# Optimization experiments

Measured on AMD Instinct MI355X. Metric: run time of the kernel, lower is better.

## Reference

```python
import jax, jax.numpy as jnp
import numpy as np

B, T, D = 2, 2048, 2048
H, DH, DR, DL = 16, 128, 64, 512
WINDOW, STRIDE, GLOBAL = 512, 64, 128
BASE, MAX_SEQ, ORIG_MAX = 10000.0, 131072, 4096
BETA_FAST, BETA_SLOW = 32.0, 1.0
SCALE = 1.0 / np.sqrt(DH)
SCALE_ROPE = 1.0 / np.sqrt(DR)


def _yarn_inv_freq():
    base_inv = 1.0 / (BASE ** (np.arange(0, DR, 2, dtype=np.float32) / DR))
    scale = MAX_SEQ / ORIG_MAX
    freqs = np.arange(DR // 2, dtype=np.float32)
    ramp = np.clip((freqs - BETA_SLOW) / (BETA_FAST - BETA_SLOW), 0.0, 1.0)
    return jnp.asarray(base_inv * (1 - ramp) + (base_inv / scale) * ramp)

_INV_FREQ = _yarn_inv_freq()
_YARN_FACTOR = np.float32(0.1 * np.log(MAX_SEQ / ORIG_MAX) + 1.0)


def _apply_rope(x):
    # x: [B, H, T, DR]
    t = jnp.arange(x.shape[2], dtype=jnp.float32)
    fr = t[:, None] * _INV_FREQ[None, :]            # [T, DR/2]
    emb = jnp.concatenate([fr, fr], axis=-1)        # [T, DR]
    cos, sin = jnp.cos(emb), jnp.sin(emb)
    x1, x2 = jnp.split(x, 2, axis=-1)
    rot = jnp.concatenate([-x2, x1], axis=-1)
    return (x * cos + rot * sin) * _YARN_FACTOR


def _sparse_mask(seq_len):
    pos = jnp.arange(seq_len)
    qp, kp = pos[:, None], pos[None, :]
    dist = qp - kp
    half = WINDOW // 2
    window = (dist >= -half) & (dist <= half)
    dilated = (kp % STRIDE == 0) | (kp < GLOBAL)
    causal = kp <= qp
    return (window | dilated) & causal              # [T, T] bool


def setup_inputs() -> dict:
    key = jax.random.key(0)
    ks = jax.random.split(key, 9)
    s = 0.02
    return {
        "x": jax.random.normal(ks[0], (B, T, D), jnp.float32),
        "w_q": jax.random.normal(ks[1], (D, D), jnp.float32) * s,
        "w_dkv": jax.random.normal(ks[2], (D, DL), jnp.float32) * s,
        "w_uk": jax.random.normal(ks[3], (DL, D), jnp.float32) * s,
        "w_uv": jax.random.normal(ks[4], (DL, D), jnp.float32) * s,
        "w_q_pos": jax.random.normal(ks[5], (D, H * DR), jnp.float32) * s,
        "w_k_pos": jax.random.normal(ks[6], (D, H * DR), jnp.float32) * s,
        "w_o": jax.random.normal(ks[7], (D, D), jnp.float32) * s,
    }


def reference(x, w_q, w_dkv, w_uk, w_uv, w_q_pos, w_k_pos, w_o):
    b, t, _ = x.shape
    # MLA projections
    q_c = (x @ w_q).reshape(b, t, H, DH).transpose(0, 2, 1, 3)      # [B,H,T,DH]
    c_kv = x @ w_dkv                                                # [B,T,DL]
    k_c = (c_kv @ w_uk).reshape(b, t, H, DH).transpose(0, 2, 1, 3)
    v_c = (c_kv @ w_uv).reshape(b, t, H, DH).transpose(0, 2, 1, 3)
    # decoupled RoPE branch (YaRN)
    q_r = (x @ w_q_pos).reshape(b, t, H, DR).transpose(0, 2, 1, 3)
    k_r = (x @ w_k_pos).reshape(b, t, H, DR).transpose(0, 2, 1, 3)
    q_r = _apply_rope(q_r)
    k_r = _apply_rope(k_r)
    # combined content + positional scores
    scores = jnp.einsum("bhqd,bhkd->bhqk", q_c, k_c) * SCALE \
           + jnp.einsum("bhqr,bhkr->bhqk", q_r, k_r) * SCALE_ROPE
    mask = _sparse_mask(t)                                          # [T,T]
    scores = jnp.where(mask[None, None], scores, -jnp.inf)
    attn = jax.nn.softmax(scores, axis=-1)
    out = jnp.einsum("bhqk,bhkd->bhqd", attn, v_c)                  # [B,H,T,DH]
    out = out.transpose(0, 2, 1, 3).reshape(b, t, D)
    return out @ w_o
```

## Files before the change

kernel.cpp:

```cpp
#include <hip/hip_runtime.h>
#include <hip/hip_bf16.h>
#include <cstdint>

typedef __attribute__((ext_vector_type(8))) short short8_t;
typedef __attribute__((ext_vector_type(4))) short short4_t;
typedef __attribute__((ext_vector_type(4))) float f32x4_t;

#define AS1 __attribute__((address_space(1)))
#define AS3 __attribute__((address_space(3)))

__device__ __forceinline__ void gload_lds16(const void* g, void* l) {
  __builtin_amdgcn_global_load_lds((const AS1 void*)g, (AS3 void*)l, 16, 0, 0);
}

__device__ __forceinline__ short8_t ld8(const __hip_bfloat16* p) {
  return *(const short8_t*)p;
}

__global__ __launch_bounds__(256) void k_prep(
    const float* __restrict__ x, __hip_bfloat16* __restrict__ xb,
    const float* __restrict__ wq,  const float* __restrict__ wqp,
    const float* __restrict__ wkp, const float* __restrict__ wdkv,
    const float* __restrict__ wuk, const float* __restrict__ wuv,
    const float* __restrict__ wo,
    __hip_bfloat16* __restrict__ Bt1, __hip_bfloat16* __restrict__ Bt2,
    __hip_bfloat16* __restrict__ woT) {
  __shared__ float t[64][65];
  int bid = blockIdx.x;
  if (bid < 4096) {
    int i = (bid * 256 + threadIdx.x) * 8;
    union { short8_t v; __hip_bfloat16 h[8]; } u;
#pragma unroll
    for (int j = 0; j < 8; ++j) u.h[j] = __float2bfloat16(x[i + j]);
    *(short8_t*)(xb + i) = u.v;
    return;
  }
  bid -= 4096;
  const float* in; __hip_bfloat16* out; int R, C, tile;
  if (bid < 1024)      { in = wq;   out = Bt1;                 R = 2048; C = 2048; tile = bid; }
  else if (bid < 1536) { in = wqp;  out = Bt1 + 2048UL * 2048; R = 2048; C = 1024; tile = bid - 1024; }
  else if (bid < 2048) { in = wkp;  out = Bt1 + 3072UL * 2048; R = 2048; C = 1024; tile = bid - 1536; }
  else if (bid < 2304) { in = wdkv; out = Bt1 + 4096UL * 2048; R = 2048; C = 512;  tile = bid - 2048; }
  else if (bid < 2560) { in = wuk;  out = Bt2;                 R = 512;  C = 2048; tile = bid - 2304; }
  else if (bid < 2816) { in = wuv;  out = Bt2 + 2048UL * 512;  R = 512;  C = 2048; tile = bid - 2560; }
  else                 { in = wo;   out = woT;                 R = 2048; C = 2048; tile = bid - 2816; }
  int nct = C >> 6;
  int ct = tile % nct, rt = tile / nct;
  int r0 = rt << 6, c0 = ct << 6;
#pragma unroll
  for (int i = 0; i < 16; ++i) {
    int idx = i * 256 + threadIdx.x;
    int r = idx >> 6, c = idx & 63;
    t[r][c] = in[(size_t)(r0 + r) * C + c0 + c];
  }
  __syncthreads();
#pragma unroll
  for (int i = 0; i < 16; ++i) {
    int idx = i * 256 + threadIdx.x;
    int c = idx >> 6, r = idx & 63;
    out[(size_t)(c0 + c) * R + r0 + r] = __float2bfloat16(t[r][c]);
  }
}

template<int MODE>
__global__ __launch_bounds__(256) void k_gemm2(const __hip_bfloat16* __restrict__ A,
                                               const __hip_bfloat16* __restrict__ Bt,
                                               int K, int nbx,
                                               void* __restrict__ O0, void* __restrict__ O1,
                                               void* __restrict__ O2, void* __restrict__ O3,
                                               float alpha) {
  __shared__ __align__(16) __hip_bfloat16 Al[3][128 * 32];
  __shared__ __align__(16) __hip_bfloat16 Bl[3][128 * 32];
  int bx = blockIdx.x % nbx, by = blockIdx.x / nbx;
  int tid = threadIdx.x, lane = tid & 63, w = tid >> 6;
  int L = lane & 15, hi = lane >> 4;
  int wr = (w >> 1) << 6, wc = (w & 1) << 6;
  f32x4_t acc[4][4] = {};
  const __hip_bfloat16* Ag = A + (size_t)(by * 128) * K;
  const __hip_bfloat16* Bg = Bt + (size_t)(bx * 128) * K;
  int rA = w * 16 + (lane >> 2);
  int cA = ((lane & 3) ^ ((lane >> 3) & 3)) * 8;
  int NT = K >> 5;

  auto stage = [&](int s) {
    int j = s % 3;
    int k0 = s << 5;
    gload_lds16(Ag + (size_t)rA * K + k0 + cA,        &Al[j][(w * 16) * 32]);
    gload_lds16(Ag + (size_t)(rA + 64) * K + k0 + cA, &Al[j][(64 + w * 16) * 32]);
    gload_lds16(Bg + (size_t)rA * K + k0 + cA,        &Bl[j][(w * 16) * 32]);
    gload_lds16(Bg + (size_t)(rA + 64) * K + k0 + cA, &Bl[j][(64 + w * 16) * 32]);
  };

  stage(0); stage(1);
  asm volatile("s_waitcnt vmcnt(4)\ns_barrier" ::: "memory");

  int hs = hi ^ ((L >> 1) & 3);
  for (int t = 0; t < NT; ++t) {
    int j = t % 3;
    short8_t af[4], bf[4];
#pragma unroll
    for (int m = 0; m < 4; ++m) af[m] = ld8(&Al[j][(wr + 16 * m + L) * 32 + 8 * hs]);
#pragma unroll
    for (int n = 0; n < 4; ++n) bf[n] = ld8(&Bl[j][(wc + 16 * n + L) * 32 + 8 * hs]);
    if (t + 2 < NT) stage(t + 2);
    __builtin_amdgcn_s_setprio(1);
#pragma unroll
    for (int m = 0; m < 4; ++m)
#pragma unroll
      for (int n = 0; n < 4; ++n)
        acc[m][n] = __builtin_amdgcn_mfma_f32_16x16x32_bf16(af[m], bf[n], acc[m][n], 0, 0, 0);
    __builtin_amdgcn_s_setprio(0);
    if (t + 2 < NT)      asm volatile("s_waitcnt vmcnt(4)\ns_barrier" ::: "memory");
    else if (t + 1 < NT) asm volatile("s_waitcnt vmcnt(0)\ns_barrier" ::: "memory");
  }

  int r0 = by * 128 + wr + 4 * hi;
  int cb = bx * 128 + wc;

  if (MODE == 1) {
    float* C = (float*)O0;
    size_t N = (size_t)nbx << 7;
#pragma unroll
    for (int m = 0; m < 4; ++m)
#pragma unroll
      for (int n = 0; n < 4; ++n)
#pragma unroll
        for (int i = 0; i < 4; ++i)
          C[(size_t)(r0 + 16 * m + i) * N + cb + 16 * n + L] = acc[m][n][i] * alpha;
  } else if (MODE == 2) {
    __hip_bfloat16* qcb = (__hip_bfloat16*)O0;
    __hip_bfloat16* qrb = (__hip_bfloat16*)O1;
    __hip_bfloat16* krb = (__hip_bfloat16*)O2;
    __hip_bfloat16* ckv = (__hip_bfloat16*)O3;
    if (bx < 16) {
      const float SCALE = 0.08838834764831845f;
#pragma unroll
      for (int m = 0; m < 4; ++m)
#pragma unroll
        for (int n = 0; n < 4; ++n)
#pragma unroll
          for (int i = 0; i < 4; ++i)
            qcb[(size_t)(r0 + 16 * m + i) * 2048 + cb + 16 * n + L] =
                __float2bfloat16(acc[m][n][i] * SCALE);
    } else if (bx < 32) {
      bool isq = bx < 24;
      __hip_bfloat16* dst = isq ? qrb : krb;
      float osc = isq ? 0.16832169878499666f : 1.3465735902799727f;
      int cbl = cb - (isq ? 2048 : 3072);
      float invf[2];
#pragma unroll
      for (int p = 0; p < 2; ++p) {
        float fi = (float)(16 * p + L);
        float bi = __expf(fi * -0.28782313662425574f);
        float ramp = fminf(fmaxf((fi - 1.0f) * (1.0f / 31.0f), 0.0f), 1.0f);
        invf[p] = bi * (1.0f - ramp * (31.0f / 32.0f));
      }
#pragma unroll
      for (int m = 0; m < 4; ++m)
#pragma unroll
        for (int i = 0; i < 4; ++i) {
          int row = r0 + 16 * m + i;
          float ft = (float)(row & 2047);
#pragma unroll
          for (int p = 0; p < 2; ++p) {
            float sn, cs;
            __sincosf(ft * invf[p], &sn, &cs);
            float x1 = acc[m][p][i], x2 = acc[m][p + 2][i];
            dst[(size_t)row * 1024 + cbl + 16 * p + L] =
                __float2bfloat16((x1 * cs - x2 * sn) * osc);
            dst[(size_t)row * 1024 + cbl + 32 + 16 * p + L] =
                __float2bfloat16((x2 * cs + x1 * sn) * osc);
          }
        }
    } else {
      int cbl = cb - 4096;
#pragma unroll
      for (int m = 0; m < 4; ++m)
#pragma unroll
        for (int n = 0; n < 4; ++n)
#pragma unroll
          for (int i = 0; i < 4; ++i)
            ckv[(size_t)(r0 + 16 * m + i) * 512 + cbl + 16 * n + L] =
                __float2bfloat16(acc[m][n][i]);
    }
  } else if (MODE == 3) {
    __hip_bfloat16* kcb = (__hip_bfloat16*)O0;
    __hip_bfloat16* vcb = (__hip_bfloat16*)O1;
    __hip_bfloat16* vT  = (__hip_bfloat16*)O2;
    if (bx < 16) {
#pragma unroll
      for (int m = 0; m < 4; ++m)
#pragma unroll
        for (int n = 0; n < 4; ++n)
#pragma unroll
          for (int i = 0; i < 4; ++i)
            kcb[(size_t)(r0 + 16 * m + i) * 2048 + cb + 16 * n + L] =
                __float2bfloat16(acc[m][n][i]);
    } else {
#pragma unroll
      for (int m = 0; m < 4; ++m)
#pragma unroll
        for (int n = 0; n < 4; ++n) {
          int vcol = cb - 2048 + 16 * n + L;
          int hh = vcol >> 7, dh = vcol & 127;
          int row0 = r0 + 16 * m;
          int b = row0 >> 11, t0 = row0 & 2047;
          union { short4_t v; __hip_bfloat16 h4[4]; } pk;
#pragma unroll
          for (int i = 0; i < 4; ++i) {
            __hip_bfloat16 bv = __float2bfloat16(acc[m][n][i]);
            vcb[(size_t)(row0 + i) * 2048 + vcol] = bv;
            pk.h4[i] = bv;
          }
          *(short4_t*)(vT + ((size_t)((b * 16 + hh) * 128 + dh) * 2048 + t0)) = pk.v;
        }
    }
  }
}

__global__ __launch_bounds__(256) void k_attn(const __hip_bfloat16* __restrict__ qc,
                                              const __hip_bfloat16* __restrict__ kc,
                                              const __hip_bfloat16* __restrict__ vcb,
                                              const __hip_bfloat16* __restrict__ qr,
                                              const __hip_bfloat16* __restrict__ kr,
                                              const __hip_bfloat16* __restrict__ vT,
                                              __hip_bfloat16* __restrict__ ao) {
  const int T = 2048;
  int bid = blockIdx.x;
  int xcd = bid & 7, r = bid >> 3;
  int jg = r >> 5;
  int qt = 31 - (r & 31);
  int bh = xcd + 8 * jg;
  int b = bh >> 4, h = bh & 15;
  int tid = threadIdx.x, lane = tid & 63, w = tid >> 6;
  int L = lane & 15, hi = lane >> 4;
  int q0 = qt * 64;

  __shared__ __align__(16) __hip_bfloat16 Kl[64 * 200];
  __shared__ __align__(16) __hip_bfloat16 Vt[128 * 64];
  __shared__ __align__(16) __hip_bfloat16 Pl[4][16 * 72];

  char* Vtb = (char*)Vt;
  const __hip_bfloat16* vTb = vT + (size_t)(b * 16 + h) * 128 * 2048;

  int qrow = q0 + w * 16 + L;
  size_t qb = (size_t)b * T + qrow;
  short8_t qf[6];
#pragma unroll
  for (int c = 0; c < 4; ++c)
    qf[c] = ld8(qc + qb * 2048 + h * 128 + 32 * c + 8 * hi);
#pragma unroll
  for (int c = 0; c < 2; ++c)
    qf[4 + c] = ld8(qr + qb * 1024 + h * 64 + 32 * c + 8 * hi);

  f32x4_t oacc[8] = {};
  float lpart[4] = {0.0f, 0.0f, 0.0f, 0.0f};

  int nd = qt - 6;

  for (int step = 0; step <= qt + 1; ++step) {
    bool compact = (step == qt + 1);
    if (compact && nd <= 0) break;
    int kt = step;
    if (!compact && kt > 1 && kt < qt - 4) continue;
    int k0 = kt * 64;

    if (!compact) {
#pragma unroll
      for (int i = 0; i < 6; ++i) {
        int ch = i * 256 + tid;
        int rr = ch / 24;
        int d = (ch % 24) * 8;
        size_t krow = (size_t)b * T + k0 + rr;
        const __hip_bfloat16* src = (d < 128)
            ? kc + krow * 2048 + h * 128 + d
            : kr + krow * 1024 + h * 64 + (d - 128);
        *(short8_t*)(Kl + rr * 200 + d) = ld8(src);
      }
#pragma unroll
      for (int i = 0; i < 4; ++i) {
        int ch = i * 256 + tid;
        int row = ch >> 3, c = ch & 7;
        int swc = c ^ (row & 7);
        *(short8_t*)(Vtb + row * 128 + 16 * swc) = ld8(vTb + (size_t)row * 2048 + k0 + c * 8);
      }
    } else {
#pragma unroll
      for (int i = 0; i < 6; ++i) {
        int ch = i * 256 + tid;
        int rr = ch / 24;
        int d = (ch % 24) * 8;
        int srcr = (rr < nd) ? 64 * (2 + rr) : 0;
        size_t krow = (size_t)b * T + srcr;
        const __hip_bfloat16* src = (d < 128)
            ? kc + krow * 2048 + h * 128 + d
            : kr + krow * 1024 + h * 64 + (d - 128);
        *(short8_t*)(Kl + rr * 200 + d) = ld8(src);
      }
#pragma unroll
      for (int i = 0; i < 2; ++i) {
        int ch = i * 256 + tid;
        int jj = ch >> 4, d0 = (ch & 15) * 8;
        if (jj < nd) {
          union { short8_t v; __hip_bfloat16 hh[8]; } u;
          u.v = ld8(vcb + (size_t)(b * 2048 + 64 * (2 + jj)) * 2048 + h * 128 + d0);
#pragma unroll
          for (int qq = 0; qq < 8; ++qq) {
            int dh = d0 + qq;
            int swc = (jj >> 3) ^ (dh & 7);
            *(__hip_bfloat16*)(Vtb + dh * 128 + 16 * swc + 2 * (jj & 7)) = u.hh[qq];
          }
        }
      }
    }
    __syncthreads();

    f32x4_t sacc[4] = {};
    __builtin_amdgcn_s_setprio(1);
#pragma unroll
    for (int n = 0; n < 4; ++n)
#pragma unroll
      for (int c = 0; c < 6; ++c) {
        short8_t bfr = ld8(Kl + (16 * n + L) * 200 + 32 * c + 8 * hi);
        sacc[n] = __builtin_amdgcn_mfma_f32_16x16x32_bf16(qf[c], bfr, sacc[n], 0, 0, 0);
      }
    __builtin_amdgcn_s_setprio(0);

    int rbase = q0 + w * 16 + 4 * hi;
#pragma unroll
    for (int n = 0; n < 4; ++n) {
      int col = L + 16 * n;
      int k = k0 + col;
#pragma unroll
      for (int i = 0; i < 4; ++i) {
        int rq = rbase + i;
        bool ok = compact ? (col < nd)
                          : ((k <= rq) && ((rq - k <= 256) || ((k & 63) == 0) || (k < 128)));
        float e = ok ? __expf(sacc[n][i]) : 0.0f;
        lpart[i] += e;
        Pl[w][(4 * hi + i) * 72 + 16 * n + L] = __float2bfloat16(e);
      }
    }

    __builtin_amdgcn_s_setprio(1);
#pragma unroll
    for (int ks = 0; ks < 2; ++ks) {
      short8_t pa = ld8(Pl[w] + L * 72 + 32 * ks + 8 * hi);
#pragma unroll
      for (int n = 0; n < 8; ++n) {
        int vrow = 16 * n + L;
        int chunk = (4 * ks + hi) ^ (vrow & 7);
        short8_t bv = *(const short8_t*)(Vtb + vrow * 128 + 16 * chunk);
        oacc[n] = __builtin_amdgcn_mfma_f32_16x16x32_bf16(pa, bv, oacc[n], 0, 0, 0);
      }
    }
    __builtin_amdgcn_s_setprio(0);
    __syncthreads();
  }

  for (int d = 1; d < 16; d <<= 1)
#pragma unroll
    for (int i = 0; i < 4; ++i) lpart[i] += __shfl_xor(lpart[i], d, 64);

#pragma unroll
  for (int n = 0; n < 8; ++n)
#pragma unroll
    for (int i = 0; i < 4; ++i) {
      int rq = q0 + w * 16 + 4 * hi + i;
      int cdh = 16 * n + L;
      float v = oacc[n][i] / lpart[i];
      ao[((size_t)b * T + rq) * 2048 + h * 128 + cdh] = __float2bfloat16(v);
    }
}

extern "C" void kernel_launch(void* const* d_in, const int* in_sizes, int n_in,
                              void* d_out, int out_size, void* d_ws, size_t ws_size,
                              hipStream_t stream) {
  const float* x     = (const float*)d_in[0];
  const float* w_q   = (const float*)d_in[1];
  const float* w_dkv = (const float*)d_in[2];
  const float* w_uk  = (const float*)d_in[3];
  const float* w_uv  = (const float*)d_in[4];
  const float* w_qp  = (const float*)d_in[5];
  const float* w_kp  = (const float*)d_in[6];
  const float* w_o   = (const float*)d_in[7];
  float* out = (float*)d_out;

  char* ws = (char*)d_ws;
  size_t off = 0;
  auto alloc = [&](size_t elems) {
    __hip_bfloat16* p = (__hip_bfloat16*)(ws + off);
    off += ((elems * 2 + 255) & ~(size_t)255);
    return p;
  };
  __hip_bfloat16* xb  = alloc(8388608);
  __hip_bfloat16* Bt1 = alloc(4608UL * 2048);
  __hip_bfloat16* Bt2 = alloc(4096UL * 512);
  __hip_bfloat16* woT = alloc(4194304);
  __hip_bfloat16* qcb = alloc(8388608);
  __hip_bfloat16* ckv = alloc(2097152);
  __hip_bfloat16* kcb = alloc(8388608);
  __hip_bfloat16* vcb = alloc(8388608);
  __hip_bfloat16* qrb = alloc(4194304);
  __hip_bfloat16* krb = alloc(4194304);
  __hip_bfloat16* aob = alloc(8388608);
  __hip_bfloat16* vT  = alloc(8388608);

  k_prep<<<7936, 256, 0, stream>>>(x, xb, w_q, w_qp, w_kp, w_dkv, w_uk, w_uv, w_o,
                                   Bt1, Bt2, woT);

  k_gemm2<2><<<36 * 32, 256, 0, stream>>>(xb, Bt1, 2048, 36, qcb, qrb, krb, ckv, 1.0f);
  k_gemm2<3><<<32 * 32, 256, 0, stream>>>(ckv, Bt2, 512, 32, kcb, vcb, vT, nullptr, 1.0f);

  k_attn<<<1024, 256, 0, stream>>>(qcb, kcb, vcb, qrb, krb, vT, aob);

  k_gemm2<1><<<16 * 32, 256, 0, stream>>>(aob, woT, 2048, 16, out, nullptr, nullptr, nullptr, 1.0f);
}
```

Measured before the change: 254.7 us.

## Use 256x256 tiles for projection GEMMs and split the c_kv GEMM out

Adds a k_gemm8 kernel with 512 threads and 256x256 output tiles, where each wave computes 128x64, and uses it for the fused Q/RoPE projection and the K/V up-projection. The c_kv down-projection is split into its own small 128x128-tile launch, so the big projection GEMM now covers an even 4096 columns. Larger tiles raise arithmetic intensity and cut redundant global loads of A and B. The cost is fewer blocks per launch (256), an extra kernel launch, more LDS and registers, and possible under-use of the GPU's CUs.

```diff
diff --git a/kernel.cpp b/kernel.cpp
--- a/kernel.cpp
+++ b/kernel.cpp
@@ -66,9 +66,7 @@
 __global__ __launch_bounds__(256) void k_gemm2(const __hip_bfloat16* __restrict__ A,
                                                const __hip_bfloat16* __restrict__ Bt,
                                                int K, int nbx,
-                                               void* __restrict__ O0, void* __restrict__ O1,
-                                               void* __restrict__ O2, void* __restrict__ O3,
-                                               float alpha) {
+                                               void* __restrict__ O0, float alpha) {
   __shared__ __align__(16) __hip_bfloat16 Al[3][128 * 32];
   __shared__ __align__(16) __hip_bfloat16 Bl[3][128 * 32];
   int bx = blockIdx.x % nbx, by = blockIdx.x / nbx;
@@ -115,35 +113,101 @@
   }
 
   int r0 = by * 128 + wr + 4 * hi;
-  int cb = bx * 128 + wc;
-
+  int c0 = bx * 128 + wc;
+  size_t N = (size_t)nbx << 7;
   if (MODE == 1) {
     float* C = (float*)O0;
-    size_t N = (size_t)nbx << 7;
 #pragma unroll
     for (int m = 0; m < 4; ++m)
 #pragma unroll
       for (int n = 0; n < 4; ++n)
 #pragma unroll
         for (int i = 0; i < 4; ++i)
-          C[(size_t)(r0 + 16 * m + i) * N + cb + 16 * n + L] = acc[m][n][i] * alpha;
-  } else if (MODE == 2) {
+          C[(size_t)(r0 + 16 * m + i) * N + c0 + 16 * n + L] = acc[m][n][i] * alpha;
+  } else {
+    __hip_bfloat16* C = (__hip_bfloat16*)O0;
+#pragma unroll
+    for (int m = 0; m < 4; ++m)
+#pragma unroll
+      for (int n = 0; n < 4; ++n)
+#pragma unroll
+        for (int i = 0; i < 4; ++i)
+          C[(size_t)(r0 + 16 * m + i) * N + c0 + 16 * n + L] =
+              __float2bfloat16(acc[m][n][i] * alpha);
+  }
+}
+
+template<int MODE>
+__global__ __launch_bounds__(512, 2) void k_gemm8(const __hip_bfloat16* __restrict__ A,
+                                                  const __hip_bfloat16* __restrict__ Bt,
+                                                  int K, int nbx,
+                                                  void* __restrict__ O0, void* __restrict__ O1,
+                                                  void* __restrict__ O2) {
+  __shared__ __align__(16) __hip_bfloat16 Al[3][256 * 32];
+  __shared__ __align__(16) __hip_bfloat16 Bl[3][256 * 32];
+  int bx = blockIdx.x % nbx, by = blockIdx.x / nbx;
+  int tid = threadIdx.x, lane = tid & 63, w = tid >> 6;
+  int L = lane & 15, hi = lane >> 4;
+  int wr = (w >> 2) << 7;
+  int wc = (w & 3) << 6;
+  f32x4_t acc[8][4] = {};
+  const __hip_bfloat16* Ag = A + (size_t)(by * 256) * K;
+  const __hip_bfloat16* Bg = Bt + (size_t)(bx * 256) * K;
+  int rA = w * 16 + (lane >> 2);
+  int cA = ((lane & 3) ^ ((lane >> 3) & 3)) * 8;
+  int NT = K >> 5;
+
+  auto stage = [&](int s) {
+    int j = s % 3;
+    int k0 = s << 5;
+    gload_lds16(Ag + (size_t)rA * K + k0 + cA,         &Al[j][(w * 16) * 32]);
+    gload_lds16(Ag + (size_t)(rA + 128) * K + k0 + cA, &Al[j][(128 + w * 16) * 32]);
+    gload_lds16(Bg + (size_t)rA * K + k0 + cA,         &Bl[j][(w * 16) * 32]);
+    gload_lds16(Bg + (size_t)(rA + 128) * K + k0 + cA, &Bl[j][(128 + w * 16) * 32]);
+  };
+
+  stage(0); stage(1);
+  asm volatile("s_waitcnt vmcnt(4)\ns_barrier" ::: "memory");
+
+  int hs = hi ^ ((L >> 1) & 3);
+  for (int t = 0; t < NT; ++t) {
+    int j = t % 3;
+    short8_t af[8], bf[4];
+#pragma unroll
+    for (int m = 0; m < 8; ++m) af[m] = ld8(&Al[j][(wr + 16 * m + L) * 32 + 8 * hs]);
+#pragma unroll
+    for (int n = 0; n < 4; ++n) bf[n] = ld8(&Bl[j][(wc + 16 * n + L) * 32 + 8 * hs]);
+    if (t + 2 < NT) stage(t + 2);
+    __builtin_amdgcn_s_setprio(1);
+#pragma unroll
+    for (int m = 0; m < 8; ++m)
+#pragma unroll
+      for (int n = 0; n < 4; ++n)
+        acc[m][n] = __builtin_amdgcn_mfma_f32_16x16x32_bf16(af[m], bf[n], acc[m][n], 0, 0, 0);
+    __builtin_amdgcn_s_setprio(0);
+    if (t + 2 < NT)      asm volatile("s_waitcnt vmcnt(4)\ns_barrier" ::: "memory");
+    else if (t + 1 < NT) asm volatile("s_waitcnt vmcnt(0)\ns_barrier" ::: "memory");
+  }
+
+  int r0 = by * 256 + wr + 4 * hi;
+  int cb = bx * 256 + wc;
+
+  if (MODE == 2) {
     __hip_bfloat16* qcb = (__hip_bfloat16*)O0;
     __hip_bfloat16* qrb = (__hip_bfloat16*)O1;
     __hip_bfloat16* krb = (__hip_bfloat16*)O2;
-    __hip_bfloat16* ckv = (__hip_bfloat16*)O3;
-    if (bx < 16) {
+    if (cb < 2048) {
       const float SCALE = 0.08838834764831845f;
 #pragma unroll
-      for (int m = 0; m < 4; ++m)
+      for (int m = 0; m < 8; ++m)
 #pragma unroll
         for (int n = 0; n < 4; ++n)
 #pragma unroll
           for (int i = 0; i < 4; ++i)
             qcb[(size_t)(r0 + 16 * m + i) * 2048 + cb + 16 * n + L] =
                 __float2bfloat16(acc[m][n][i] * SCALE);
-    } else if (bx < 32) {
-      bool isq = bx < 24;
+    } else {
+      bool isq = cb < 3072;
       __hip_bfloat16* dst = isq ? qrb : krb;
       float osc = isq ? 0.16832169878499666f : 1.3465735902799727f;
       int cbl = cb - (isq ? 2048 : 3072);
@@ -156,7 +220,7 @@
         invf[p] = bi * (1.0f - ramp * (31.0f / 32.0f));
       }
 #pragma unroll
-      for (int m = 0; m < 4; ++m)
+      for (int m = 0; m < 8; ++m)
 #pragma unroll
         for (int i = 0; i < 4; ++i) {
           int row = r0 + 16 * m + i;
@@ -172,24 +236,14 @@
                 __float2bfloat16((x2 * cs + x1 * sn) * osc);
           }
         }
-    } else {
-      int cbl = cb - 4096;
-#pragma unroll
-      for (int m = 0; m < 4; ++m)
-#pragma unroll
-        for (int n = 0; n < 4; ++n)
-#pragma unroll
-          for (int i = 0; i < 4; ++i)
-            ckv[(size_t)(r0 + 16 * m + i) * 512 + cbl + 16 * n + L] =
-                __float2bfloat16(acc[m][n][i]);
     }
   } else if (MODE == 3) {
     __hip_bfloat16* kcb = (__hip_bfloat16*)O0;
     __hip_bfloat16* vcb = (__hip_bfloat16*)O1;
     __hip_bfloat16* vT  = (__hip_bfloat16*)O2;
-    if (bx < 16) {
-#pragma unroll
-      for (int m = 0; m < 4; ++m)
+    if (cb < 2048) {
+#pragma unroll
+      for (int m = 0; m < 8; ++m)
 #pragma unroll
         for (int n = 0; n < 4; ++n)
 #pragma unroll
@@ -198,7 +252,7 @@
                 __float2bfloat16(acc[m][n][i]);
     } else {
 #pragma unroll
-      for (int m = 0; m < 4; ++m)
+      for (int m = 0; m < 8; ++m)
 #pragma unroll
         for (int n = 0; n < 4; ++n) {
           int vcol = cb - 2048 + 16 * n + L;
@@ -409,10 +463,11 @@
   k_prep<<<7936, 256, 0, stream>>>(x, xb, w_q, w_qp, w_kp, w_dkv, w_uk, w_uv, w_o,
                                    Bt1, Bt2, woT);
 
-  k_gemm2<2><<<36 * 32, 256, 0, stream>>>(xb, Bt1, 2048, 36, qcb, qrb, krb, ckv, 1.0f);
-  k_gemm2<3><<<32 * 32, 256, 0, stream>>>(ckv, Bt2, 512, 32, kcb, vcb, vT, nullptr, 1.0f);
+  k_gemm2<4><<<4 * 32, 256, 0, stream>>>(xb, Bt1 + 4096UL * 2048, 2048, 4, ckv, 1.0f);
+  k_gemm8<2><<<16 * 16, 512, 0, stream>>>(xb, Bt1, 2048, 16, qcb, qrb, krb);
+  k_gemm8<3><<<16 * 16, 512, 0, stream>>>(ckv, Bt2, 512, 16, kcb, vcb, vT);
 
   k_attn<<<1024, 256, 0, stream>>>(qcb, kcb, vcb, qrb, krb, vT, aob);
 
-  k_gemm2<1><<<16 * 32, 256, 0, stream>>>(aob, woT, 2048, 16, out, nullptr, nullptr, nullptr, 1.0f);
-}
+  k_gemm2<1><<<16 * 32, 256, 0, stream>>>(aob, woT, 2048, 16, out, 1.0f);
+}
```

New measurement: 253.6 us. About the same (-0.4%).
